# Optimization experiments

Hardware: AMD Instinct MI355X
Metric: run time of the kernel (lower is better)

## Reference

```python
import jax, jax.numpy as jnp
import numpy as np

B, T, D, U = 32, 4096, 512, 256

def setup_inputs() -> dict:
    key = jax.random.key(0)
    ks = jax.random.split(key, 5)
    s = 1.0 / np.sqrt(D)
    return {
        "values": jax.random.normal(ks[0], (B, T, D), dtype=jnp.float32),
        "query": jax.random.normal(ks[1], (B, D), dtype=jnp.float32),
        "W1": jax.random.normal(ks[2], (D, U), dtype=jnp.float32) * s,
        "b1": jnp.zeros((U,), dtype=jnp.float32),
        "W2": jax.random.normal(ks[3], (D, U), dtype=jnp.float32) * s,
        "b2": jnp.zeros((U,), dtype=jnp.float32),
        "V": jax.random.normal(ks[4], (U, 1), dtype=jnp.float32) * (1.0 / np.sqrt(U)),
        "bV": jnp.zeros((1,), dtype=jnp.float32),
    }

def reference(values, query, W1, b1, W2, b2, V, bV):
    # values: [B,T,D], query: [B,D]
    h_vals = jnp.einsum('btd,du->btu', values, W1) + b1          # [B,T,U]
    h_query = (query @ W2 + b2)[:, None, :]                       # [B,1,U]
    score = jnp.einsum('btu,uo->bto', jnp.tanh(h_vals + h_query), V) + bV  # [B,T,1]
    attention_weights = jax.nn.softmax(score, axis=1)             # [B,T,1]
    context_vector = jnp.sum(attention_weights * values, axis=1)  # [B,D]
    return context_vector, attention_weights
```

## Files before the change

### kernel.cpp

```cpp
#include <hip/hip_runtime.h>
#include <math.h>
#include <stdint.h>

#define BB 32
#define TT 4096
#define DD 512
#define UU 256

#define KC 32
#define NKC (DD/KC)
#define LDB 40
#define NTILE (TT/64)

typedef __attribute__((ext_vector_type(8))) short short8;
typedef __attribute__((ext_vector_type(8))) unsigned short ushort8;
typedef __attribute__((ext_vector_type(4))) float floatx4;

typedef const __attribute__((address_space(1))) unsigned int GU32;
typedef __attribute__((address_space(3))) unsigned int LU32;

__device__ __forceinline__ unsigned short bf16_rne(float x) {
  union { float f; uint32_t u; } v; v.f = x;
  uint32_t r = v.u + 0x7FFFu + ((v.u >> 16) & 1u);
  return (unsigned short)(r >> 16);
}
__device__ __forceinline__ float tanh_fast(float x) {
  float e = __expf(2.0f * x);
  return 1.0f - 2.0f * __builtin_amdgcn_rcpf(e + 1.0f);
}

__global__ __launch_bounds__(256) void prep_w1_kernel(
    const float* __restrict__ W1, unsigned short* __restrict__ staged) {
  const int kc = blockIdx.x;
  const int u = threadIdx.x;
  __attribute__((aligned(16))) unsigned short row[LDB];
#pragma unroll
  for (int kk = 0; kk < KC; ++kk)
    row[kk] = bf16_rne(W1[(kc * KC + kk) * UU + u]);
#pragma unroll
  for (int kk = KC; kk < LDB; ++kk) row[kk] = 0;
  unsigned short* dst = staged + ((size_t)kc * UU + u) * LDB;
#pragma unroll
  for (int i = 0; i < 5; ++i) ((uint4*)dst)[i] = *(const uint4*)&row[i * 8];
}

__global__ __launch_bounds__(256) void hquery_kernel(
    const float* __restrict__ query, const float* __restrict__ W2,
    const float* __restrict__ b2, const float* __restrict__ b1,
    float* __restrict__ hq) {
  const int b = blockIdx.x;
  const int u = threadIdx.x;
  __shared__ float qs[DD];
  for (int d = threadIdx.x; d < DD; d += 256) qs[d] = query[b * DD + d];
  __syncthreads();
  float acc = b2[u] + b1[u];
  for (int d = 0; d < DD; ++d) acc += qs[d] * W2[d * UU + u];
  hq[b * UU + u] = acc;
}

__global__ __launch_bounds__(256) void score_kernel(
    const float* __restrict__ values, const unsigned short* __restrict__ w1s,
    const float* __restrict__ hq, const float* __restrict__ V,
    const float* __restrict__ bV, float* __restrict__ scores,
    float* __restrict__ pml, float* __restrict__ pctx) {
  const int b = blockIdx.y;
  const int blk = blockIdx.x;
  const int t0 = blk * 64;
  const int tid = threadIdx.x;
  const int wave = tid >> 6;
  const int lane = tid & 63;
  const int c = lane & 15;
  const int q = lane >> 4;

  __shared__ unsigned short As[64 * LDB];
  __shared__ unsigned short Bs[UU * LDB];
  __shared__ float redW[4][64];
  __shared__ float warr[64];

  floatx4 acc[4][4];
#pragma unroll
  for (int ti = 0; ti < 4; ++ti)
#pragma unroll
    for (int ui = 0; ui < 4; ++ui) acc[ti][ui] = (floatx4){0.f, 0.f, 0.f, 0.f};

  const int ar = tid >> 2;
  const int aseg = tid & 3;
  const float* asrc =
      values + ((size_t)b * TT + t0) * DD + (size_t)ar * DD + aseg * 8;

  float4 a0 = *(const float4*)asrc;
  float4 a1 = *(const float4*)(asrc + 4);

  for (int kc = 0; kc < NKC; ++kc) {
    __syncthreads();
    {
      ushort8 t8;
      t8[0] = bf16_rne(a0.x); t8[1] = bf16_rne(a0.y);
      t8[2] = bf16_rne(a0.z); t8[3] = bf16_rne(a0.w);
      t8[4] = bf16_rne(a1.x); t8[5] = bf16_rne(a1.y);
      t8[6] = bf16_rne(a1.z); t8[7] = bf16_rne(a1.w);
      *(ushort8*)&As[ar * LDB + aseg * 8] = t8;
    }
    {
      GU32* src = (GU32*)(w1s + (size_t)kc * UU * LDB);
      LU32* dst = (LU32*)Bs;
#pragma unroll
      for (int i = 0; i < 5; ++i)
        __builtin_amdgcn_global_load_lds(src + (i * 256 + tid) * 4,
                                         dst + (i * 256 + tid) * 4, 16, 0, 0);
    }
    __syncthreads();

    short8 afr[4], bfr[4];
#pragma unroll
    for (int ti = 0; ti < 4; ++ti)
      afr[ti] = *(const short8*)&As[(ti * 16 + c) * LDB + q * 8];
#pragma unroll
    for (int ui = 0; ui < 4; ++ui)
      bfr[ui] = *(const short8*)&Bs[(wave * 64 + ui * 16 + c) * LDB + q * 8];
#pragma unroll
    for (int ti = 0; ti < 4; ++ti)
#pragma unroll
      for (int ui = 0; ui < 4; ++ui)
        acc[ti][ui] = __builtin_amdgcn_mfma_f32_16x16x32_bf16(
            afr[ti], bfr[ui], acc[ti][ui], 0, 0, 0);

    if (kc + 1 < NKC) {
      a0 = *(const float4*)(asrc + (kc + 1) * KC);
      a1 = *(const float4*)(asrc + (kc + 1) * KC + 4);
    }
  }

  float hqv[4], vv[4];
#pragma unroll
  for (int ui = 0; ui < 4; ++ui) {
    const int u = wave * 64 + ui * 16 + c;
    hqv[ui] = hq[b * UU + u];
    vv[ui] = V[u];
  }
#pragma unroll
  for (int ti = 0; ti < 4; ++ti)
#pragma unroll
    for (int r = 0; r < 4; ++r) {
      float e = 0.0f;
#pragma unroll
      for (int ui = 0; ui < 4; ++ui)
        e += tanh_fast(acc[ti][ui][r] + hqv[ui]) * vv[ui];
      e += __shfl_xor(e, 1, 64);
      e += __shfl_xor(e, 2, 64);
      e += __shfl_xor(e, 4, 64);
      e += __shfl_xor(e, 8, 64);
      if (c == 0) redW[wave][ti * 16 + q * 4 + r] = e;
    }
  __syncthreads();
  if (tid < 64) {
    const float s =
        bV[0] + redW[0][tid] + redW[1][tid] + redW[2][tid] + redW[3][tid];
    scores[b * TT + t0 + tid] = s;
    redW[0][tid] = s;
  }
  __syncthreads();
  float mb = -1e30f;
#pragma unroll 8
  for (int t = 0; t < 64; ++t) mb = fmaxf(mb, redW[0][t]);
  if (tid < 64) warr[tid] = __expf(redW[0][tid] - mb);
  __syncthreads();
  float lb = 0.0f;
#pragma unroll 8
  for (int t = 0; t < 64; ++t) lb += warr[t];

  const float2* vp = (const float2*)(values + ((size_t)b * TT + t0) * DD);
  float2 c2 = {0.f, 0.f};
#pragma unroll 4
  for (int t = 0; t < 64; ++t) {
    const float w = warr[t];
    const float2 v = vp[(size_t)t * (DD / 2) + tid];
    c2.x += w * v.x;
    c2.y += w * v.y;
  }
  *(float2*)&pctx[((size_t)b * NTILE + blk) * DD + 2 * tid] = c2;
  if (tid == 0) {
    pml[(b * NTILE + blk) * 2 + 0] = mb;
    pml[(b * NTILE + blk) * 2 + 1] = lb;
  }
}

__global__ __launch_bounds__(256) void combine_kernel(
    const float* __restrict__ pml, const float* __restrict__ pctx,
    float* __restrict__ out, float* __restrict__ stats) {
  const int b = blockIdx.x;
  const int tid = threadIdx.x;
  __shared__ float mls[2 * NTILE];
  __shared__ float cs[NTILE];
  if (tid < 2 * NTILE) mls[tid] = pml[b * 2 * NTILE + tid];
  __syncthreads();
  float m = -1e30f;
#pragma unroll 8
  for (int i = 0; i < NTILE; ++i) m = fmaxf(m, mls[2 * i]);
  if (tid < NTILE) cs[tid] = __expf(mls[2 * tid] - m);
  __syncthreads();
  float l = 0.0f;
#pragma unroll 8
  for (int i = 0; i < NTILE; ++i) l += cs[i] * mls[2 * i + 1];

  const float2* pp = (const float2*)(pctx + (size_t)b * NTILE * DD);
  float2 acc = {0.f, 0.f};
#pragma unroll 4
  for (int i = 0; i < NTILE; ++i) {
    const float cw = cs[i];
    const float2 p = pp[(size_t)i * (DD / 2) + tid];
    acc.x += cw * p.x;
    acc.y += cw * p.y;
  }
  const float linv = 1.0f / l;
  out[b * DD + 2 * tid + 0] = acc.x * linv;
  out[b * DD + 2 * tid + 1] = acc.y * linv;
  if (tid == 0) {
    stats[2 * b + 0] = m;
    stats[2 * b + 1] = l;
  }
}

__global__ __launch_bounds__(256) void weights_kernel(
    const float* __restrict__ scores, const float* __restrict__ stats,
    float* __restrict__ out) {
  const int b = blockIdx.y;
  const int t = blockIdx.x * 256 + threadIdx.x;
  const float m = stats[2 * b];
  const float linv = 1.0f / stats[2 * b + 1];
  out[BB * DD + b * TT + t] = __expf(scores[b * TT + t] - m) * linv;
}

extern "C" void kernel_launch(void* const* d_in, const int* in_sizes, int n_in,
                              void* d_out, int out_size, void* d_ws, size_t ws_size,
                              hipStream_t stream) {
  const float* values = (const float*)d_in[0];
  const float* query  = (const float*)d_in[1];
  const float* W1     = (const float*)d_in[2];
  const float* b1     = (const float*)d_in[3];
  const float* W2     = (const float*)d_in[4];
  const float* b2     = (const float*)d_in[5];
  const float* V      = (const float*)d_in[6];
  const float* bV     = (const float*)d_in[7];
  float* out = (float*)d_out;

  float* ws = (float*)d_ws;
  float* hq     = ws;
  float* scores = ws + BB * UU;
  float* stats  = scores + BB * TT;
  float* pml    = stats + 2 * BB;
  float* pctx   = pml + BB * NTILE * 2;
  unsigned short* w1s = (unsigned short*)(pctx + (size_t)BB * NTILE * DD);

  prep_w1_kernel<<<NKC, 256, 0, stream>>>(W1, w1s);
  hquery_kernel<<<BB, 256, 0, stream>>>(query, W2, b2, b1, hq);
  score_kernel<<<dim3(NTILE, BB), 256, 0, stream>>>(
      values, w1s, hq, V, bV, scores, pml, pctx);
  combine_kernel<<<BB, 256, 0, stream>>>(pml, pctx, out, stats);
  weights_kernel<<<dim3(TT / 256, BB), 256, 0, stream>>>(scores, stats, out);
}
```

Measured before the change: 461.7 us.

## Load W1 fragments directly from global and double-buffer the A tile in LDS

The W1 B-operand is no longer staged through LDS with global_load_lds. Each wave now reads its bf16 MFMA fragments straight from a compact, unpadded global layout that should stay cache-resident. The A tile gets a two-slot LDS buffer, so one barrier per K-chunk replaces two, and values are prefetched two chunks ahead in registers. This cuts LDS traffic, LDS size and synchronisation, at the cost of per-wave global loads for B, more live registers, and a dependence on L2 hits for W1.

```diff
diff --git a/kernel.cpp b/kernel.cpp
--- a/kernel.cpp
+++ b/kernel.cpp
@@ -9,15 +9,12 @@
 
 #define KC 32
 #define NKC (DD/KC)
-#define LDB 40
+#define LDA 40
 #define NTILE (TT/64)
 
 typedef __attribute__((ext_vector_type(8))) short short8;
 typedef __attribute__((ext_vector_type(8))) unsigned short ushort8;
 typedef __attribute__((ext_vector_type(4))) float floatx4;
-
-typedef const __attribute__((address_space(1))) unsigned int GU32;
-typedef __attribute__((address_space(3))) unsigned int LU32;
 
 __device__ __forceinline__ unsigned short bf16_rne(float x) {
   union { float f; uint32_t u; } v; v.f = x;
@@ -30,18 +27,16 @@
 }
 
 __global__ __launch_bounds__(256) void prep_w1_kernel(
-    const float* __restrict__ W1, unsigned short* __restrict__ staged) {
+    const float* __restrict__ W1, unsigned short* __restrict__ w1t) {
   const int kc = blockIdx.x;
   const int u = threadIdx.x;
-  __attribute__((aligned(16))) unsigned short row[LDB];
+  __attribute__((aligned(16))) unsigned short row[KC];
 #pragma unroll
   for (int kk = 0; kk < KC; ++kk)
     row[kk] = bf16_rne(W1[(kc * KC + kk) * UU + u]);
-#pragma unroll
-  for (int kk = KC; kk < LDB; ++kk) row[kk] = 0;
-  unsigned short* dst = staged + ((size_t)kc * UU + u) * LDB;
-#pragma unroll
-  for (int i = 0; i < 5; ++i) ((uint4*)dst)[i] = *(const uint4*)&row[i * 8];
+  unsigned short* dst = w1t + ((size_t)kc * UU + u) * KC;
+#pragma unroll
+  for (int i = 0; i < 4; ++i) ((uint4*)dst)[i] = *(const uint4*)&row[i * 8];
 }
 
 __global__ __launch_bounds__(256) void hquery_kernel(
@@ -59,7 +54,7 @@
 }
 
 __global__ __launch_bounds__(256) void score_kernel(
-    const float* __restrict__ values, const unsigned short* __restrict__ w1s,
+    const float* __restrict__ values, const unsigned short* __restrict__ w1t,
     const float* __restrict__ hq, const float* __restrict__ V,
     const float* __restrict__ bV, float* __restrict__ scores,
     float* __restrict__ pml, float* __restrict__ pctx) {
@@ -72,8 +67,7 @@
   const int c = lane & 15;
   const int q = lane >> 4;
 
-  __shared__ unsigned short As[64 * LDB];
-  __shared__ unsigned short Bs[UU * LDB];
+  __shared__ unsigned short As[2][64 * LDA];
   __shared__ float redW[4][64];
   __shared__ float warr[64];
 
@@ -86,49 +80,49 @@
   const int ar = tid >> 2;
   const int aseg = tid & 3;
   const float* asrc =
-      values + ((size_t)b * TT + t0) * DD + (size_t)ar * DD + aseg * 8;
-
-  float4 a0 = *(const float4*)asrc;
-  float4 a1 = *(const float4*)(asrc + 4);
+      values + ((size_t)b * TT + t0 + ar) * DD + aseg * 8;
+
+  const unsigned short* bbase = w1t + ((size_t)(wave * 64 + c)) * KC + q * 8;
+
+  float4 aq[2][2];
+  aq[0][0] = *(const float4*)(asrc);
+  aq[0][1] = *(const float4*)(asrc + 4);
+  aq[1][0] = *(const float4*)(asrc + KC);
+  aq[1][1] = *(const float4*)(asrc + KC + 4);
 
   for (int kc = 0; kc < NKC; ++kc) {
-    __syncthreads();
+    const int buf = kc & 1;
     {
+      const float4 f0 = aq[buf][0], f1 = aq[buf][1];
       ushort8 t8;
-      t8[0] = bf16_rne(a0.x); t8[1] = bf16_rne(a0.y);
-      t8[2] = bf16_rne(a0.z); t8[3] = bf16_rne(a0.w);
-      t8[4] = bf16_rne(a1.x); t8[5] = bf16_rne(a1.y);
-      t8[6] = bf16_rne(a1.z); t8[7] = bf16_rne(a1.w);
-      *(ushort8*)&As[ar * LDB + aseg * 8] = t8;
-    }
-    {
-      GU32* src = (GU32*)(w1s + (size_t)kc * UU * LDB);
-      LU32* dst = (LU32*)Bs;
-#pragma unroll
-      for (int i = 0; i < 5; ++i)
-        __builtin_amdgcn_global_load_lds(src + (i * 256 + tid) * 4,
-                                         dst + (i * 256 + tid) * 4, 16, 0, 0);
+      t8[0] = bf16_rne(f0.x); t8[1] = bf16_rne(f0.y);
+      t8[2] = bf16_rne(f0.z); t8[3] = bf16_rne(f0.w);
+      t8[4] = bf16_rne(f1.x); t8[5] = bf16_rne(f1.y);
+      t8[6] = bf16_rne(f1.z); t8[7] = bf16_rne(f1.w);
+      *(ushort8*)&As[buf][ar * LDA + aseg * 8] = t8;
     }
     __syncthreads();
 
-    short8 afr[4], bfr[4];
+    short8 bfr[4];
+#pragma unroll
+    for (int ui = 0; ui < 4; ++ui)
+      bfr[ui] = *(const short8*)(bbase + ((size_t)kc * UU + ui * 16) * KC);
+    short8 afr[4];
 #pragma unroll
     for (int ti = 0; ti < 4; ++ti)
-      afr[ti] = *(const short8*)&As[(ti * 16 + c) * LDB + q * 8];
-#pragma unroll
-    for (int ui = 0; ui < 4; ++ui)
-      bfr[ui] = *(const short8*)&Bs[(wave * 64 + ui * 16 + c) * LDB + q * 8];
+      afr[ti] = *(const short8*)&As[buf][(ti * 16 + c) * LDA + q * 8];
+
+    if (kc + 2 < NKC) {
+      aq[buf][0] = *(const float4*)(asrc + (kc + 2) * KC);
+      aq[buf][1] = *(const float4*)(asrc + (kc + 2) * KC + 4);
+    }
+
 #pragma unroll
     for (int ti = 0; ti < 4; ++ti)
 #pragma unroll
       for (int ui = 0; ui < 4; ++ui)
         acc[ti][ui] = __builtin_amdgcn_mfma_f32_16x16x32_bf16(
             afr[ti], bfr[ui], acc[ti][ui], 0, 0, 0);
-
-    if (kc + 1 < NKC) {
-      a0 = *(const float4*)(asrc + (kc + 1) * KC);
-      a1 = *(const float4*)(asrc + (kc + 1) * KC + 4);
-    }
   }
 
   float hqv[4], vv[4];
@@ -250,12 +244,12 @@
   float* stats  = scores + BB * TT;
   float* pml    = stats + 2 * BB;
   float* pctx   = pml + BB * NTILE * 2;
-  unsigned short* w1s = (unsigned short*)(pctx + (size_t)BB * NTILE * DD);
-
-  prep_w1_kernel<<<NKC, 256, 0, stream>>>(W1, w1s);
+  unsigned short* w1t = (unsigned short*)(pctx + (size_t)BB * NTILE * DD);
+
+  prep_w1_kernel<<<NKC, 256, 0, stream>>>(W1, w1t);
   hquery_kernel<<<BB, 256, 0, stream>>>(query, W2, b2, b1, hq);
   score_kernel<<<dim3(NTILE, BB), 256, 0, stream>>>(
-      values, w1s, hq, V, bV, scores, pml, pctx);
+      values, w1t, hq, V, bV, scores, pml, pctx);
   combine_kernel<<<BB, 256, 0, stream>>>(pml, pctx, out, stats);
   weights_kernel<<<dim3(TT / 256, BB), 256, 0, stream>>>(scores, stats, out);
 }
```

Result: no change. 456.9 us (-1.0%).
